# Kernel tuning notes

Hardware: AMD Instinct MI355X
Metric: run time of the kernel (lower is better)

Reference implementation:

```python
import jax, jax.numpy as jnp
import numpy as np

EMBED_DIM = 1024
NUM_HEADS = 16
HEAD_DIM = EMBED_DIM // NUM_HEADS
WINDOW = 256


def setup_inputs() -> dict:
    key = jax.random.key(0)
    ks = jax.random.split(key, 9)
    B, S, E = 4, 4096, EMBED_DIM
    sc = 1.0 / np.sqrt(E)
    return {
        "x": jax.random.normal(ks[0], (B, S, E), jnp.float32),
        "Wq": jax.random.normal(ks[1], (E, E), jnp.float32) * sc,
        "bq": jax.random.normal(ks[2], (E,), jnp.float32) * 0.01,
        "Wk": jax.random.normal(ks[3], (E, E), jnp.float32) * sc,
        "bk": jax.random.normal(ks[4], (E,), jnp.float32) * 0.01,
        "Wv": jax.random.normal(ks[5], (E, E), jnp.float32) * sc,
        "bv": jax.random.normal(ks[6], (E,), jnp.float32) * 0.01,
        "Wo": jax.random.normal(ks[7], (E, E), jnp.float32) * sc,
        "bo": jax.random.normal(ks[8], (E,), jnp.float32) * 0.01,
    }


def reference(x, Wq, bq, Wk, bk, Wv, bv, Wo, bo):
    B, S, E = x.shape
    H, D, W = NUM_HEADS, HEAD_DIM, WINDOW
    NW = S // W  # seq_len chosen divisible by window -> no padding

    def split_heads(t):  # [B,S,E] -> [B,H,NW,W,D]
        return t.reshape(B, S, H, D).transpose(0, 2, 1, 3).reshape(B, H, NW, W, D)

    q = split_heads(x @ Wq + bq)
    k = split_heads(x @ Wk + bk)
    v = split_heads(x @ Wv + bv)

    # block-diagonal attention within each non-overlapping window
    scores = jnp.einsum("bhnqd,bhnkd->bhnqk", q, k) / jnp.sqrt(
        jnp.asarray(D, x.dtype))
    attn = jax.nn.softmax(scores, axis=-1)
    out = jnp.einsum("bhnqk,bhnkd->bhnqd", attn, v)  # [B,H,NW,W,D]

    out = out.reshape(B, H, S, D).transpose(0, 2, 1, 3).reshape(B, S, E)
    return out @ Wo + bo
```

## Files before the change

### kernel.cpp

```cpp
#include <hip/hip_runtime.h>

typedef __bf16 bf16x8 __attribute__((ext_vector_type(8)));
typedef float  f32x4  __attribute__((ext_vector_type(4)));

#define MFMA(a,b,c) __builtin_amdgcn_mfma_f32_16x16x32_bf16((a),(b),(c),0,0,0)
#define SB() __builtin_amdgcn_sched_barrier(0)
#define LGKM0 asm volatile("s_waitcnt lgkmcnt(0)" ::: "memory")

__device__ __forceinline__ unsigned short f2bf(float f){
  unsigned u = __builtin_bit_cast(unsigned, f);
  u += 0x7fffu + ((u>>16)&1u);
  return (unsigned short)(u>>16);
}
__device__ __forceinline__ unsigned pack_bf2(float a, float b){
  return (unsigned)f2bf(a) | ((unsigned)f2bf(b)<<16);
}
__device__ __forceinline__ void gload_lds16(const void* g, void* l){
  __builtin_amdgcn_global_load_lds((__attribute__((address_space(1))) void*)(g),
                                   (__attribute__((address_space(3))) void*)(l), 16, 0, 0);
}

__global__ void k_cvt_x(const float* __restrict__ x, unsigned short* __restrict__ o){
  const size_t t = (size_t)blockIdx.x*256 + threadIdx.x;
  #pragma unroll
  for (int i=0;i<4;i++){
    size_t idx = t + (size_t)i*1048576;
    float4 f = ((const float4*)x)[idx];
    ((uint2*)o)[idx] = make_uint2(pack_bf2(f.x,f.y), pack_bf2(f.z,f.w));
  }
}

__global__ void k_cvt_wT(const float* __restrict__ Wq, const float* __restrict__ Wk,
                         const float* __restrict__ Wv, const float* __restrict__ Wo,
                         unsigned short* __restrict__ wT){
  const int z = blockIdx.z;
  const float* W = (z==0)?Wq:(z==1)?Wk:(z==2)?Wv:Wo;
  unsigned short* out = wT + (size_t)z*1048576;
  __shared__ float tile[32][33];
  const int r0 = blockIdx.y*32, c0 = blockIdx.x*32;
  const int r = threadIdx.x>>5, c = threadIdx.x&31;
  #pragma unroll
  for (int i=0;i<4;i++) tile[r + i*8][c] = W[(size_t)(r0 + r + i*8)*1024 + c0 + c];
  __syncthreads();
  #pragma unroll
  for (int i=0;i<4;i++)
    out[(size_t)(c0 + r + i*8)*1024 + r0 + c] = f2bf(tile[c][r + i*8]);
}

#define QUAD16(AF, BF, MF0) do { \
  _Pragma("unroll") \
  for (int mf_=0; mf_<4; ++mf_){ \
    _Pragma("unroll") \
    for (int nf_=0; nf_<4; ++nf_) \
      acc[MF0+mf_][nf_] = MFMA(AF[mf_], BF[nf_], acc[MF0+mf_][nf_]); \
  } } while(0)

#define READ_A(DST, MF0, KOFF, AB) do { \
  _Pragma("unroll") \
  for (int mf_=0; mf_<4; ++mf_) \
    DST[mf_] = *(const bf16x8*)((AB) + (((MF0)+mf_)*16+l15)*128 + (((KOFF)+g*16) ^ sw)); \
  } while(0)

#define READ_B(DST, KOFF, BB) do { \
  _Pragma("unroll") \
  for (int nf_=0; nf_<4; ++nf_) \
    DST[nf_] = *(const bf16x8*)((BB) + (brow+nf_*16+l15)*128 + (((KOFF)+g*16) ^ sw)); \
  } while(0)

template<int MODE>
__global__ __launch_bounds__(512,2) void k_gemm8(const unsigned short* __restrict__ A,
                       const unsigned short* __restrict__ Bm,
                       const float* __restrict__ bias0, const float* __restrict__ bias1,
                       const float* __restrict__ bias2,
                       unsigned short* __restrict__ q_ws, unsigned short* __restrict__ k_ws,
                       unsigned short* __restrict__ v_ws, float* __restrict__ outf)
{
  __shared__ char smem[131072];
  const int tid = threadIdx.x, lane = tid&63, wid = tid>>6;
  const int g = lane>>4, l15 = lane&15;
  const int wr = wid>>2, wc = wid&3;

  constexpr int NBX = (MODE==0)? 12 : 4;
  constexpr int CPX = (MODE==0)? 96 : 32;
  const int flat = blockIdx.y*NBX + blockIdx.x;
  const int swz  = (flat&7)*CPX + (flat>>3);
  const int m0 = (swz/NBX)<<8, n0 = (swz%NBX)<<8;

  auto stageH = [&](int isA, int tt, int hf){
    char* ldst = smem + (isA?0:65536) + (tt&1)*32768 + hf*16384 + wid*1024;
    const unsigned short* gbase = isA? A : Bm;
    const int row0 = (isA? m0 : n0) + hf*128;
    #pragma unroll
    for (int j=0;j<2;j++){
      const int o = (j*512 + tid)*16;
      const int r = o>>7, cb = o&127;
      const int cs = cb ^ ((r&7)<<4);
      gload_lds16((const char*)gbase + (size_t)(row0 + r)*2048 + (tt<<7) + cs,
                  ldst + j*8192);
    }
  };

  f32x4 acc[8][4];
  #pragma unroll
  for (int i=0;i<8;i++)
    #pragma unroll
    for (int j=0;j<4;j++) acc[i][j] = f32x4{0.f,0.f,0.f,0.f};

  const int sw = (l15&7)<<4;
  const int brow = (wc&1)*64;
  bf16x8 A0f[4], A1f[4], B0f[4], B1f[4];

  stageH(1,0,0); stageH(1,0,1);
  stageH(0,0,0); stageH(0,0,1);
  stageH(1,1,0); stageH(1,1,1);
  asm volatile("s_waitcnt vmcnt(4)" ::: "memory");
  __builtin_amdgcn_s_barrier();
  SB();
  {
    const char* Ab0 = smem + wr*16384;
    const char* Bb0 = smem + 65536 + (wc>>1)*16384;
    READ_A(A0f, 0, 0, Ab0);
    READ_B(B0f, 0, Bb0);
  }

  #pragma unroll 1
  for (int t=0;t<16;++t){
    const char* Abc = smem + (t&1)*32768 + wr*16384;
    const char* Bbc = smem + 65536 + (t&1)*32768 + (wc>>1)*16384;
    const char* Abn = smem + ((t+1)&1)*32768 + wr*16384;
    const char* Bbn = smem + 65536 + ((t+1)&1)*32768 + (wc>>1)*16384;

    LGKM0; SB();
    __builtin_amdgcn_s_barrier(); SB();
    READ_A(A1f, 4, 0, Abc);
    if (t+1 < 16) stageH(0, t+1, 0);
    SB();
    __builtin_amdgcn_s_setprio(1);
    QUAD16(A0f, B0f, 0);
    __builtin_amdgcn_s_setprio(0);
    SB();

    LGKM0; SB();
    __builtin_amdgcn_s_barrier(); SB();
    READ_A(A0f, 0, 64, Abc);
    READ_B(B1f, 64, Bbc);
    if (t+1 < 16) stageH(0, t+1, 1);
    SB();
    __builtin_amdgcn_s_setprio(1);
    QUAD16(A1f, B0f, 4);
    __builtin_amdgcn_s_setprio(0);
    SB();

    LGKM0; SB();
    __builtin_amdgcn_s_barrier(); SB();
    READ_A(A1f, 4, 64, Abc);
    SB();
    __builtin_amdgcn_s_setprio(1);
    QUAD16(A0f, B1f, 0);
    __builtin_amdgcn_s_setprio(0);
    SB();

    LGKM0; SB();
    __builtin_amdgcn_s_barrier(); SB();
    if (t+2 < 16){ stageH(1, t+2, 0); stageH(1, t+2, 1); }
    if (t+1 < 16){
      if (t+2 < 16) asm volatile("s_waitcnt vmcnt(4)" ::: "memory");
      else          asm volatile("s_waitcnt vmcnt(0)" ::: "memory");
    }
    __builtin_amdgcn_s_barrier(); SB();
    if (t+1 < 16){
      READ_A(A0f, 0, 0, Abn);
      READ_B(B0f, 0, Bbn);
    }
    SB();
    __builtin_amdgcn_s_setprio(1);
    QUAD16(A1f, B1f, 4);
    __builtin_amdgcn_s_setprio(0);
    SB();
  }

  if constexpr (MODE==0){
    const int z  = n0>>10;
    const int nE = n0 & 1023;
    const float* bias = (z==0)? bias0 : (z==1)? bias1 : bias2;
    #pragma unroll
    for (int nf=0;nf<4;nf++){
      const int ncol = nE + wc*64 + nf*16 + l15;
      const float bn = bias[ncol];
      const int h = ncol>>6, d = ncol&63;
      #pragma unroll
      for (int mf=0;mf<8;mf++){
        const int mb = m0 + wr*128 + mf*16 + g*4;
        if (z==2){
          const int b = mb>>12, s = mb&4095, nw = s>>8, w0 = s&255;
          unsigned short pk0=f2bf(acc[mf][nf][0]+bn), pk1=f2bf(acc[mf][nf][1]+bn),
                         pk2=f2bf(acc[mf][nf][2]+bn), pk3=f2bf(acc[mf][nf][3]+bn);
          size_t idx = ((((size_t)(b*16+h)*16 + nw)*64 + d)<<8) + w0;
          *(ushort4*)(v_ws + idx) = make_ushort4(pk0,pk1,pk2,pk3);
        } else {
          unsigned short* dst = (z==0)? q_ws : k_ws;
          const float scale = (z==0)? 0.125f : 1.0f;
          #pragma unroll
          for (int r=0;r<4;r++){
            const int m = mb + r, b = m>>12, s = m&4095;
            dst[(((size_t)(b*16+h)*4096 + s)<<6) + d] = f2bf((acc[mf][nf][r]+bn)*scale);
          }
        }
      }
    }
  } else {
    #pragma unroll
    for (int nf=0;nf<4;nf++){
      const int n = n0 + wc*64 + nf*16 + l15;
      const float bn = bias0[n];
      #pragma unroll
      for (int mf=0;mf<8;mf++)
        #pragma unroll
        for (int r=0;r<4;r++){
          const int m = m0 + wr*128 + mf*16 + g*4 + r;
          outf[(size_t)m*1024 + n] = acc[mf][nf][r] + bn;
        }
    }
  }
}

__global__ __launch_bounds__(256,2) void k_attn(const unsigned short* __restrict__ qw,
                                                const unsigned short* __restrict__ kw,
                                                const unsigned short* __restrict__ vw,
                                                unsigned short* __restrict__ ow)
{
  __shared__ unsigned short Ks[2][4096];
  __shared__ unsigned short Vs[2][4096];
  __shared__ unsigned short Ps[4][4096];
  const int tid = threadIdx.x, lane = tid&63, wid = tid>>6;
  const int g = lane>>4, l15 = lane&15;
  const int bhn = blockIdx.x;
  const int nw = bhn&15, h = (bhn>>4)&15, b = bhn>>8;

  const size_t qkbase = ((size_t)((b*16+h)*4096 + nw*256))<<6;
  const unsigned short* Qg = qw + qkbase;
  const unsigned short* Kg = kw + qkbase;
  const unsigned short* Vg = vw + (((size_t)(b*16+h)*16 + nw)<<14);
  const float NEG_INF = -__builtin_inff();

  bf16x8 qa[4][2];
  #pragma unroll
  for (int qf=0;qf<4;qf++)
    #pragma unroll
    for (int ks=0;ks<2;ks++)
      qa[qf][ks] = *(const bf16x8*)((const char*)Qg + (wid*64 + qf*16 + l15)*128 + ks*64 + g*16);

  auto stage = [&](int kt, int bi){
    #pragma unroll
    for (int i=0;i<4;i++){
      const int chunk = wid*4 + i;
      const int obase = (chunk&7)<<10;
      const int o = obase + lane*16;
      const int r = o>>7, cb = o&127;
      const int cs = cb ^ ((r&7)<<4);
      if (chunk < 8)
        gload_lds16((const char*)Kg + (kt*64 + r)*128 + cs, (char*)Ks[bi] + obase);
      else
        gload_lds16((const char*)Vg + r*512 + kt*128 + cs, (char*)Vs[bi] + obase);
    }
  };

  f32x4 oacc[4][4];
  float mrow[4][4], lrow[4][4];
  #pragma unroll
  for (int i=0;i<4;i++)
    #pragma unroll
    for (int j=0;j<4;j++){ oacc[i][j] = f32x4{0.f,0.f,0.f,0.f}; mrow[i][j] = NEG_INF; lrow[i][j] = 0.f; }

  stage(0,0);
  __syncthreads();
  for (int kt=0;kt<4;kt++){
    const int cur = kt&1;
    if (kt<3) stage(kt+1, cur^1);

    bf16x8 kb[4][2];
    #pragma unroll
    for (int kf=0;kf<4;kf++)
      #pragma unroll
      for (int ks=0;ks<2;ks++){
        const int kr = kf*16 + l15, cb = ks*64 + g*16;
        kb[kf][ks] = *(const bf16x8*)((const char*)Ks[cur] + kr*128 + (cb ^ ((kr&7)<<4)));
      }

    unsigned short* P = Ps[wid];
    #pragma unroll
    for (int qf=0;qf<4;qf++){
      f32x4 sfr[4];
      #pragma unroll
      for (int kf=0;kf<4;kf++){
        f32x4 zz = f32x4{0.f,0.f,0.f,0.f};
        zz = MFMA(qa[qf][0], kb[kf][0], zz);
        sfr[kf] = MFMA(qa[qf][1], kb[kf][1], zz);
      }
      #pragma unroll
      for (int r=0;r<4;r++){
        float t = fmaxf(fmaxf(sfr[0][r],sfr[1][r]), fmaxf(sfr[2][r],sfr[3][r]));
        t = fmaxf(t, __shfl_xor(t,1,64)); t = fmaxf(t, __shfl_xor(t,2,64));
        t = fmaxf(t, __shfl_xor(t,4,64)); t = fmaxf(t, __shfl_xor(t,8,64));
        const float mo = mrow[qf][r];
        const float mn = fmaxf(mo, t);
        const float alpha = __expf(mo - mn);
        float rs = 0.f;
        #pragma unroll
        for (int kf=0;kf<4;kf++){ float p = __expf(sfr[kf][r]-mn); sfr[kf][r] = p; rs += p; }
        rs += __shfl_xor(rs,1,64); rs += __shfl_xor(rs,2,64);
        rs += __shfl_xor(rs,4,64); rs += __shfl_xor(rs,8,64);
        lrow[qf][r] = lrow[qf][r]*alpha + rs;
        mrow[qf][r] = mn;
        #pragma unroll
        for (int df=0;df<4;df++) oacc[qf][df][r] *= alpha;
        const int prow = qf*16 + g*4 + r;
        const int sw = (prow&7)<<4;
        char* Pb = (char*)P + prow*128;
        #pragma unroll
        for (int kf=0;kf<4;kf++)
          *(unsigned short*)(Pb + (((kf*16 + l15)*2) ^ sw)) = f2bf(sfr[kf][r]);
      }
    }
    __builtin_amdgcn_sched_barrier(0);

    bf16x8 vb[4][2];
    #pragma unroll
    for (int df=0;df<4;df++)
      #pragma unroll
      for (int ks=0;ks<2;ks++){
        const int d = df*16 + l15, cb = ks*64 + g*16;
        vb[df][ks] = *(const bf16x8*)((const char*)Vs[cur] + d*128 + (cb ^ ((d&7)<<4)));
      }
    #pragma unroll
    for (int qf=0;qf<4;qf++){
      const int pr = qf*16 + l15;
      const bf16x8 pa0 = *(const bf16x8*)((const char*)P + pr*128 + ((g*16)      ^ ((pr&7)<<4)));
      const bf16x8 pa1 = *(const bf16x8*)((const char*)P + pr*128 + ((64 + g*16) ^ ((pr&7)<<4)));
      #pragma unroll
      for (int df=0;df<4;df++){
        oacc[qf][df] = MFMA(pa0, vb[df][0], oacc[qf][df]);
        oacc[qf][df] = MFMA(pa1, vb[df][1], oacc[qf][df]);
      }
    }
    __syncthreads();
  }

  #pragma unroll
  for (int qf=0;qf<4;qf++)
    #pragma unroll
    for (int r=0;r<4;r++){
      const float inv = 1.f / lrow[qf][r];
      const int srow = nw*256 + wid*64 + qf*16 + g*4 + r;
      const size_t base = ((size_t)b*4096 + srow)*1024 + (size_t)h*64;
      #pragma unroll
      for (int df=0;df<4;df++)
        ow[base + df*16 + l15] = f2bf(oacc[qf][df][r]*inv);
    }
}

extern "C" void kernel_launch(void* const* d_in, const int* in_sizes, int n_in,
                              void* d_out, int out_size, void* d_ws, size_t ws_size,
                              hipStream_t stream)
{
  const float* x  = (const float*)d_in[0];
  const float* Wq = (const float*)d_in[1];
  const float* bq = (const float*)d_in[2];
  const float* Wk = (const float*)d_in[3];
  const float* bk = (const float*)d_in[4];
  const float* Wv = (const float*)d_in[5];
  const float* bv = (const float*)d_in[6];
  const float* Wo = (const float*)d_in[7];
  const float* bo = (const float*)d_in[8];
  float* out = (float*)d_out;

  char* ws = (char*)d_ws;
  unsigned short* xbf  = (unsigned short*)(ws);
  unsigned short* wT   = (unsigned short*)(ws + (size_t)32*1048576);
  unsigned short* q_ws = (unsigned short*)(ws + (size_t)40*1048576);
  unsigned short* k_ws = (unsigned short*)(ws + (size_t)72*1048576);
  unsigned short* v_ws = (unsigned short*)(ws + (size_t)104*1048576);
  unsigned short* obf  = xbf;

  k_cvt_x<<<4096,256,0,stream>>>(x, xbf);
  k_cvt_wT<<<dim3(32,32,4),256,0,stream>>>(Wq,Wk,Wv,Wo, wT);
  k_gemm8<0><<<dim3(12,64),512,0,stream>>>(xbf, wT, bq,bk,bv, q_ws,k_ws,v_ws, nullptr);
  k_attn<<<1024,256,0,stream>>>(q_ws,k_ws,v_ws, obf);
  k_gemm8<1><<<dim3(4,64),512,0,stream>>>(obf, wT + (size_t)3*1048576, bo,nullptr,nullptr,
                                          nullptr,nullptr,nullptr, out);
}
```

Baseline: 263.0 us.

## Restructure GEMM main loop into 8-phase half-tile staged pipeline with new tile mapping

Rewrites the bf16 GEMM main loop as an unrolled sequence of eight phases per two k-steps. Each phase reads one A/B fragment set from LDS and issues one half-tile global-to-LDS stage, which spreads the loads evenly across the MFMA phases and halves the fragment registers held at once. It also replaces the 2D grid swizzle with a 1D mapping that groups eight consecutive M tiles per XCD slot, aimed at better L2 reuse. In exchange it adds a barrier in every phase and uses a tighter vmcnt wait scheme that must exactly match the staging order.

```diff
diff --git a/kernel.cpp b/kernel.cpp
--- a/kernel.cpp
+++ b/kernel.cpp
@@ -6,6 +6,7 @@
 #define MFMA(a,b,c) __builtin_amdgcn_mfma_f32_16x16x32_bf16((a),(b),(c),0,0,0)
 #define SB() __builtin_amdgcn_sched_barrier(0)
 #define LGKM0 asm volatile("s_waitcnt lgkmcnt(0)" ::: "memory")
+#define VMC(N) asm volatile("s_waitcnt vmcnt(" #N ")" ::: "memory")
 
 __device__ __forceinline__ unsigned short f2bf(float f){
   unsigned u = __builtin_bit_cast(unsigned, f);
@@ -66,6 +67,10 @@
   for (int nf_=0; nf_<4; ++nf_) \
     DST[nf_] = *(const bf16x8*)((BB) + (brow+nf_*16+l15)*128 + (((KOFF)+g*16) ^ sw)); \
   } while(0)
+
+#define PH_OPEN   SB(); __builtin_amdgcn_s_barrier(); LGKM0; SB(); __builtin_amdgcn_s_setprio(1)
+#define PH_CLOSE  __builtin_amdgcn_s_setprio(0); SB()
+#define PH_END    __builtin_amdgcn_s_barrier(); SB()
 
 template<int MODE>
 __global__ __launch_bounds__(512,2) void k_gemm8(const unsigned short* __restrict__ A,
@@ -80,11 +85,11 @@
   const int g = lane>>4, l15 = lane&15;
   const int wr = wid>>2, wc = wid&3;
 
-  constexpr int NBX = (MODE==0)? 12 : 4;
-  constexpr int CPX = (MODE==0)? 96 : 32;
-  const int flat = blockIdx.y*NBX + blockIdx.x;
-  const int swz  = (flat&7)*CPX + (flat>>3);
-  const int m0 = (swz/NBX)<<8, n0 = (swz%NBX)<<8;
+  constexpr int NN = (MODE==0)? 12 : 4;
+  const int x  = blockIdx.x & 7;
+  const int c  = blockIdx.x >> 3;
+  const int m0 = ((c/NN)*8 + x) << 8;
+  const int n0 = (c%NN) << 8;
 
   auto stageH = [&](int isA, int tt, int hf){
     char* ldst = smem + (isA?0:65536) + (tt&1)*32768 + hf*16384 + wid*1024;
@@ -108,75 +113,54 @@
 
   const int sw = (l15&7)<<4;
   const int brow = (wc&1)*64;
-  bf16x8 A0f[4], A1f[4], B0f[4], B1f[4];
-
-  stageH(1,0,0); stageH(1,0,1);
-  stageH(0,0,0); stageH(0,0,1);
-  stageH(1,1,0); stageH(1,1,1);
-  asm volatile("s_waitcnt vmcnt(4)" ::: "memory");
-  __builtin_amdgcn_s_barrier();
-  SB();
+  const char* Ab0 = smem + wr*16384;
+  const char* Bb0 = smem + 65536 + (wc>>1)*16384;
+  const char* Ab1 = Ab0 + 32768;
+  const char* Bb1 = Bb0 + 32768;
+  bf16x8 aF[4], bF[4];
+
+  stageH(1,0,0); stageH(1,0,1); stageH(0,0,0); stageH(0,0,1);
+  stageH(0,1,0);
+  VMC(2);
+  __builtin_amdgcn_s_barrier(); SB();
+
+  #pragma unroll 1
+  for (int i=0;i<7;++i){
+    const int T = 2*i;
+    READ_A(aF,0,0,Ab0); READ_B(bF,0,Bb0); stageH(0,T+1,1);
+    PH_OPEN; QUAD16(aF,bF,0); PH_CLOSE; PH_END;
+    READ_A(aF,4,0,Ab0); stageH(1,T+1,0);
+    PH_OPEN; QUAD16(aF,bF,4); PH_CLOSE; PH_END;
+    READ_A(aF,0,64,Ab0); READ_B(bF,64,Bb0); stageH(1,T+1,1);
+    PH_OPEN; QUAD16(aF,bF,0); PH_CLOSE; PH_END;
+    READ_A(aF,4,64,Ab0); stageH(0,T+2,0);
+    PH_OPEN; QUAD16(aF,bF,4); PH_CLOSE; VMC(2); PH_END;
+    READ_A(aF,0,0,Ab1); READ_B(bF,0,Bb1); stageH(0,T+2,1);
+    PH_OPEN; QUAD16(aF,bF,0); PH_CLOSE; PH_END;
+    READ_A(aF,4,0,Ab1); stageH(1,T+2,0);
+    PH_OPEN; QUAD16(aF,bF,4); PH_CLOSE; PH_END;
+    READ_A(aF,0,64,Ab1); READ_B(bF,64,Bb1); stageH(1,T+2,1);
+    PH_OPEN; QUAD16(aF,bF,0); PH_CLOSE; PH_END;
+    READ_A(aF,4,64,Ab1); stageH(0,T+3,0);
+    PH_OPEN; QUAD16(aF,bF,4); PH_CLOSE; VMC(2); PH_END;
+  }
   {
-    const char* Ab0 = smem + wr*16384;
-    const char* Bb0 = smem + 65536 + (wc>>1)*16384;
-    READ_A(A0f, 0, 0, Ab0);
-    READ_B(B0f, 0, Bb0);
-  }
-
-  #pragma unroll 1
-  for (int t=0;t<16;++t){
-    const char* Abc = smem + (t&1)*32768 + wr*16384;
-    const char* Bbc = smem + 65536 + (t&1)*32768 + (wc>>1)*16384;
-    const char* Abn = smem + ((t+1)&1)*32768 + wr*16384;
-    const char* Bbn = smem + 65536 + ((t+1)&1)*32768 + (wc>>1)*16384;
-
-    LGKM0; SB();
-    __builtin_amdgcn_s_barrier(); SB();
-    READ_A(A1f, 4, 0, Abc);
-    if (t+1 < 16) stageH(0, t+1, 0);
-    SB();
-    __builtin_amdgcn_s_setprio(1);
-    QUAD16(A0f, B0f, 0);
-    __builtin_amdgcn_s_setprio(0);
-    SB();
-
-    LGKM0; SB();
-    __builtin_amdgcn_s_barrier(); SB();
-    READ_A(A0f, 0, 64, Abc);
-    READ_B(B1f, 64, Bbc);
-    if (t+1 < 16) stageH(0, t+1, 1);
-    SB();
-    __builtin_amdgcn_s_setprio(1);
-    QUAD16(A1f, B0f, 4);
-    __builtin_amdgcn_s_setprio(0);
-    SB();
-
-    LGKM0; SB();
-    __builtin_amdgcn_s_barrier(); SB();
-    READ_A(A1f, 4, 64, Abc);
-    SB();
-    __builtin_amdgcn_s_setprio(1);
-    QUAD16(A0f, B1f, 0);
-    __builtin_amdgcn_s_setprio(0);
-    SB();
-
-    LGKM0; SB();
-    __builtin_amdgcn_s_barrier(); SB();
-    if (t+2 < 16){ stageH(1, t+2, 0); stageH(1, t+2, 1); }
-    if (t+1 < 16){
-      if (t+2 < 16) asm volatile("s_waitcnt vmcnt(4)" ::: "memory");
-      else          asm volatile("s_waitcnt vmcnt(0)" ::: "memory");
-    }
-    __builtin_amdgcn_s_barrier(); SB();
-    if (t+1 < 16){
-      READ_A(A0f, 0, 0, Abn);
-      READ_B(B0f, 0, Bbn);
-    }
-    SB();
-    __builtin_amdgcn_s_setprio(1);
-    QUAD16(A1f, B1f, 4);
-    __builtin_amdgcn_s_setprio(0);
-    SB();
+    READ_A(aF,0,0,Ab0); READ_B(bF,0,Bb0); stageH(0,15,1);
+    PH_OPEN; QUAD16(aF,bF,0); PH_CLOSE; PH_END;
+    READ_A(aF,4,0,Ab0); stageH(1,15,0);
+    PH_OPEN; QUAD16(aF,bF,4); PH_CLOSE; PH_END;
+    READ_A(aF,0,64,Ab0); READ_B(bF,64,Bb0); stageH(1,15,1);
+    PH_OPEN; QUAD16(aF,bF,0); PH_CLOSE; PH_END;
+    READ_A(aF,4,64,Ab0);
+    PH_OPEN; QUAD16(aF,bF,4); PH_CLOSE; VMC(0); PH_END;
+    READ_A(aF,0,0,Ab1); READ_B(bF,0,Bb1);
+    PH_OPEN; QUAD16(aF,bF,0); PH_CLOSE; PH_END;
+    READ_A(aF,4,0,Ab1);
+    PH_OPEN; QUAD16(aF,bF,4); PH_CLOSE; PH_END;
+    READ_A(aF,0,64,Ab1); READ_B(bF,64,Bb1);
+    PH_OPEN; QUAD16(aF,bF,0); PH_CLOSE; PH_END;
+    READ_A(aF,4,64,Ab1);
+    PH_OPEN; QUAD16(aF,bF,4); PH_CLOSE; PH_END;
   }
 
   if constexpr (MODE==0){
@@ -384,8 +368,8 @@
 
   k_cvt_x<<<4096,256,0,stream>>>(x, xbf);
   k_cvt_wT<<<dim3(32,32,4),256,0,stream>>>(Wq,Wk,Wv,Wo, wT);
-  k_gemm8<0><<<dim3(12,64),512,0,stream>>>(xbf, wT, bq,bk,bv, q_ws,k_ws,v_ws, nullptr);
+  k_gemm8<0><<<768,512,0,stream>>>(xbf, wT, bq,bk,bv, q_ws,k_ws,v_ws, nullptr);
   k_attn<<<1024,256,0,stream>>>(q_ws,k_ws,v_ws, obf);
-  k_gemm8<1><<<dim3(4,64),512,0,stream>>>(obf, wT + (size_t)3*1048576, bo,nullptr,nullptr,
-                                          nullptr,nullptr,nullptr, out);
-}
+  k_gemm8<1><<<256,512,0,stream>>>(obf, wT + (size_t)3*1048576, bo,nullptr,nullptr,
+                                   nullptr,nullptr,nullptr, out);
+}
```

Measured after the change: 260.6 us. No clear change (-0.9%).
